# Optimization experiments

Hardware: AMD Instinct MI355X
Metric: run time of the kernel (lower is better)

The kernel has to match this reference:

```python
import jax, jax.numpy as jnp
import numpy as np
import math

B, N, DIM, NH, K, PD = 2, 2048, 512, 8, 32, 16
HD = DIM // NH
LN_EPS = 1e-6  # flax LayerNorm default


def _poincare_dist(x, y, c):
    # x, y broadcast to [B, N, N, PD]; returns [B, N, N]
    diff_norm_sq = jnp.sum((x - y) ** 2, axis=-1)
    x_norm_sq = jnp.sum(x ** 2, axis=-1)
    y_norm_sq = jnp.sum(y ** 2, axis=-1)
    den = (1.0 - c * x_norm_sq) * (1.0 - c * y_norm_sq)
    arg = 1.0 + 2.0 * c * diff_norm_sq / jnp.clip(den, 1e-8)
    safe_arg = jnp.maximum(arg, 1.0 + 1e-7)
    return jnp.arccosh(safe_arg) / jnp.sqrt(c)


def _layernorm(x, scale, bias):
    m = jnp.mean(x, axis=-1, keepdims=True)
    v = jnp.var(x, axis=-1, keepdims=True)
    return (x - m) / jnp.sqrt(v + LN_EPS) * scale + bias


def setup_inputs() -> dict:
    key = jax.random.key(0)
    ks = jax.random.split(key, 12)

    def dense(k, din, dout):
        W = jax.random.normal(k, (din, dout), jnp.float32) / np.sqrt(din).astype(np.float32)
        b = jnp.zeros((dout,), jnp.float32)
        return W, b

    inp = {}
    inp["x"] = jax.random.normal(ks[0], (B, N, DIM), jnp.float32)
    # points inside the unit Poincare ball (c=1)
    inp["positions"] = (jax.random.uniform(ks[1], (B, N, PD), jnp.float32) - 0.5) * 0.2
    inp["c"] = jnp.float32(1.0)
    inp["Wq"], inp["bq"] = dense(ks[2], DIM, DIM)
    inp["Wk"], inp["bk"] = dense(ks[3], DIM, DIM)
    inp["Wv"], inp["bv"] = dense(ks[4], DIM, DIM)
    inp["Wo"], inp["bo"] = dense(ks[5], DIM, DIM)
    inp["W1"], inp["b1"] = dense(ks[6], DIM, 4 * DIM)
    inp["W2"], inp["b2"] = dense(ks[7], 4 * DIM, DIM)
    inp["ln1_scale"] = jnp.ones((DIM,), jnp.float32)
    inp["ln1_bias"] = jnp.zeros((DIM,), jnp.float32)
    inp["ln2_scale"] = jnp.ones((DIM,), jnp.float32)
    inp["ln2_bias"] = jnp.zeros((DIM,), jnp.float32)
    inp["log_tau"] = jnp.zeros((1,), jnp.float32)
    inp["attn_scale"] = jnp.ones((1,), jnp.float32)
    return inp


def reference(x, positions, c, Wq, bq, Wk, bk, Wv, bv, Wo, bo,
              W1, b1, W2, b2, ln1_scale, ln1_bias, ln2_scale, ln2_bias,
              log_tau, attn_scale):
    x_res = x
    x_norm = _layernorm(x, ln1_scale, ln1_bias)

    def heads(W, b):
        return (x_norm @ W + b).reshape(B, N, NH, HD).transpose(0, 2, 1, 3)  # [B,H,N,HD]

    q = heads(Wq, bq)
    k = heads(Wk, bk)
    v = heads(Wv, bv)

    # pairwise hyperbolic distances [B,N,N]
    dist_matrix = _poincare_dist(positions[:, None, :, :], positions[:, :, None, :], c)
    _, top_k_indices = jax.lax.top_k(-dist_matrix, K)  # [B,N,K]

    # gather neighbor K/V: out[b,h,i,j,d] = kv[b,h, idx[b,i,j], d]
    gather = jax.vmap(lambda kv_b, idx_b: kv_b[:, idx_b, :])
    k_gathered = gather(k, top_k_indices)  # [B,H,N,K,HD]
    v_gathered = gather(v, top_k_indices)  # [B,H,N,K,HD]

    feature_scores = jnp.einsum('bhid,bhikd->bhik', q, k_gathered) / math.sqrt(HD)
    gathered_dists = jnp.take_along_axis(dist_matrix, top_k_indices, axis=-1)  # [B,N,K]
    geometric_scores = -gathered_dists[:, None, :, :] / jnp.clip(jnp.exp(log_tau), 1e-8)
    attn_scores = attn_scale * jnp.tanh(feature_scores + geometric_scores)
    attn_weights = jax.nn.softmax(attn_scores, axis=-1)

    attn_output = jnp.einsum('bhik,bhikd->bhid', attn_weights, v_gathered)
    attn_output = attn_output.transpose(0, 2, 1, 3).reshape(B, N, DIM)

    x1 = x_res + attn_output @ Wo + bo
    x2_norm = _layernorm(x1, ln2_scale, ln2_bias)
    ffn = jax.nn.gelu(x2_norm @ W1 + b1) @ W2 + b2  # gelu approximate=True (flax default)
    return x1 + ffn
```

## Files before the change

### kernel.cpp

```cpp
#include <hip/hip_runtime.h>
#include <math.h>

#define B_   2
#define N_   2048
#define DIM_ 512
#define NH_  8
#define HD_  64
#define K_   32
#define PD_  16
#define TOK_ (B_*N_)
#define FFN_ 2048
#define QKV_ (3*DIM_)
#define KV_  1024

typedef __bf16 bf16x8 __attribute__((ext_vector_type(8)));
typedef float  f32x4  __attribute__((ext_vector_type(4)));

__device__ __forceinline__ unsigned short f2bf(float f) {
    unsigned int u = __float_as_uint(f);
    u = (u + 0x7fffu + ((u >> 16) & 1u)) >> 16;
    return (unsigned short)u;
}

__device__ __forceinline__ float bflo(unsigned u) { return __uint_as_float(u << 16); }
__device__ __forceinline__ float bfhi(unsigned u) { return __uint_as_float(u & 0xffff0000u); }

__device__ __forceinline__ float gelu_tanh(float x) {
    float x3 = x * x * x;
    return 0.5f * x * (1.f + tanhf(0.7978845608028654f * (x + 0.044715f * x3)));
}

__device__ __forceinline__ float tanh_fast(float x) {
    float e = __expf(2.f * x);
    return 1.f - 2.f / (e + 1.f);
}

__device__ __forceinline__ int lane_mbcnt(unsigned long long m) {
    return __builtin_amdgcn_mbcnt_hi((unsigned)(m >> 32),
           __builtin_amdgcn_mbcnt_lo((unsigned)m, 0));
}

#define GLOAD_LDS16(g, l) __builtin_amdgcn_global_load_lds(                        \
    (const __attribute__((address_space(1))) unsigned int*)(const void*)(g),       \
    (__attribute__((address_space(3))) unsigned int*)(void*)(l), 16, 0, 0)

template<int EPI, int BM, int BN>
__global__ __launch_bounds__(256)
void gemm_bf16_kernel(const unsigned short* __restrict__ A,
                      const unsigned short* __restrict__ Bt,
                      const float* __restrict__ bias,
                      const float* __restrict__ res,
                      float* __restrict__ Cf,
                      unsigned short* __restrict__ Cb,
                      int N, int Kstride, int Kchunk)
{
    constexpr int WM = BM / 2;
    constexpr int WN = BN / 2;
    constexpr int FM = WM / 16;
    constexpr int FN = WN / 16;

    __shared__ __align__(16) unsigned short smem[(BM+BN)*64];
    unsigned short* As_ = smem;
    unsigned short* Bs_ = smem + BM * 64;

    int t    = threadIdx.x;
    int lane = t & 63;
    int wid  = t >> 6;
    int wm   = wid >> 1, wn = wid & 1;
    int bm0  = blockIdx.y * BM;
    int bn0  = blockIdx.x * BN;
    int quad = lane >> 4;
    int rlo  = lane & 15;
    int kbase = blockIdx.z * Kchunk;

    f32x4 acc[FM][FN] = {};

    for (int k0 = kbase; k0 < kbase + Kchunk; k0 += 64) {
#pragma unroll
        for (int l = 0; l < BM/32; l++) {
            int idx = l*256 + t;
            int r   = idx >> 3;
            int g   = (idx & 7) ^ (r & 7);
            GLOAD_LDS16(A + (size_t)(bm0 + r) * Kstride + k0 + g*8, As_ + idx*8);
        }
#pragma unroll
        for (int l = 0; l < BN/32; l++) {
            int idx = l*256 + t;
            int r   = idx >> 3;
            int g   = (idx & 7) ^ (r & 7);
            GLOAD_LDS16(Bt + (size_t)(bn0 + r) * Kstride + k0 + g*8, Bs_ + idx*8);
        }
        __syncthreads();

        bf16x8 af[FM][2], bfr[FN][2];
#pragma unroll
        for (int mi = 0; mi < FM; mi++) {
            int r = wm*WM + mi*16 + rlo;
#pragma unroll
            for (int s = 0; s < 2; s++)
                af[mi][s] = *(const bf16x8*)(As_ + r*64 + ((s*4 + quad) ^ (r & 7))*8);
        }
#pragma unroll
        for (int ni = 0; ni < FN; ni++) {
            int r = wn*WN + ni*16 + rlo;
#pragma unroll
            for (int s = 0; s < 2; s++)
                bfr[ni][s] = *(const bf16x8*)(Bs_ + r*64 + ((s*4 + quad) ^ (r & 7))*8);
        }
#pragma unroll
        for (int s = 0; s < 2; s++)
#pragma unroll
            for (int mi = 0; mi < FM; mi++)
#pragma unroll
                for (int ni = 0; ni < FN; ni++)
                    acc[mi][ni] = __builtin_amdgcn_mfma_f32_16x16x32_bf16(
                        af[mi][s], bfr[ni][s], acc[mi][ni], 0, 0, 0);
        __syncthreads();
    }

#pragma unroll
    for (int mi = 0; mi < FM; mi++) {
#pragma unroll
        for (int ni = 0; ni < FN; ni++) {
            int col = bn0 + wn*WN + ni*16 + rlo;
            float bv = (EPI == 4) ? 0.f : bias[col];
#pragma unroll
            for (int r = 0; r < 4; r++) {
                int row = bm0 + wm*WM + mi*16 + quad*4 + r;
                float val = acc[mi][ni][r] + bv;
                if (EPI == 1) val += res[(size_t)row * N + col];
                if (EPI == 2) {
                    val = gelu_tanh(val);
                    Cb[(size_t)row * N + col] = f2bf(val);
                } else if (EPI == 3) {
                    if (col < DIM_) Cf[(size_t)row * DIM_ + col] = val;
                    else            Cb[(size_t)row * KV_ + (col - DIM_)] = f2bf(val);
                } else if (EPI == 4) {
                    atomicAdd(&Cf[(size_t)row * N + col], val);
                } else {
                    Cf[(size_t)row * N + col] = val;
                }
            }
        }
    }
}

__device__ __forceinline__ void extract_row(const unsigned* rb, unsigned T,
                                            int cnt_lt, int m,
                                            unsigned long long* crow,
                                            int hw, int jbase, int lane)
{
    int ltpos = 0;
#pragma unroll
    for (int tt = 0; tt < 16; tt++) {
        bool is_lt = rb[tt] < T;
        unsigned long long mlt = __ballot(is_lt);
        int p = ltpos + lane_mbcnt(mlt);
        if (is_lt) {
            int j = jbase + (tt >> 2)*256 + lane*4 + (tt & 3);
            crow[hw*K_ + p] = ((unsigned long long)rb[tt] << 32) | (unsigned)j;
        }
        ltpos += __popcll(mlt);
    }
    int eqpos = 0;
#pragma unroll
    for (int jg = 0; jg < 4; jg++) {
        bool iseq[4]; unsigned long long meq[4]; int bel[4];
#pragma unroll
        for (int jj = 0; jj < 4; jj++) {
            iseq[jj] = (rb[jg*4+jj] == T);
            meq[jj]  = __ballot(iseq[jj]);
            bel[jj]  = lane_mbcnt(meq[jj]);
        }
        int lane_prefix = bel[0] + bel[1] + bel[2] + bel[3];
        int within = 0;
#pragma unroll
        for (int jj = 0; jj < 4; jj++) {
            int p = eqpos + lane_prefix + within;
            if (iseq[jj] && p < m) {
                int j = jbase + jg*256 + lane*4 + jj;
                crow[hw*K_ + cnt_lt + p] =
                    ((unsigned long long)rb[jg*4+jj] << 32) | (unsigned)j;
            }
            within += iseq[jj] ? 1 : 0;
        }
        eqpos += __popcll(meq[0]) + __popcll(meq[1]) + __popcll(meq[2]) + __popcll(meq[3]);
    }
}

__global__ __launch_bounds__(256)
void dist_topk_kernel(const float* __restrict__ pos,
                      const float* __restrict__ posT,
                      const float* __restrict__ pos_sq,
                      const float* __restrict__ c_ptr,
                      int* __restrict__ topk_idx, float* __restrict__ topk_dist)
{
    __shared__ unsigned long long cand[4][64];

    int wid  = threadIdx.x >> 6;
    int lane = threadIdx.x & 63;
    int rg   = wid >> 1;
    int hw   = wid & 1;
    int bi0  = blockIdx.x * 4 + rg * 2;
    int b    = bi0 >> 11;
    float c  = *c_ptr;
    float inv_sqrt_c = rsqrtf(c);

    float pi0[16], pi1[16];
    {
        const float4* q0 = (const float4*)(pos + (size_t)bi0 * PD_);
        const float4* q1 = (const float4*)(pos + (size_t)(bi0+1) * PD_);
#pragma unroll
        for (int u = 0; u < 4; u++) {
            float4 a = q0[u];
            pi0[4*u]=a.x; pi0[4*u+1]=a.y; pi0[4*u+2]=a.z; pi0[4*u+3]=a.w;
            float4 e = q1[u];
            pi1[4*u]=e.x; pi1[4*u+1]=e.y; pi1[4*u+2]=e.z; pi1[4*u+3]=e.w;
        }
    }
    float om0 = 1.f - c * pos_sq[bi0];
    float om1 = 1.f - c * pos_sq[bi0+1];

    const float* pT  = posT + (size_t)b * 16 * N_;
    const float* sqb = pos_sq + b * N_;
    int jbase = hw * 1024;
    int j0l   = jbase + lane * 4;

    unsigned rb0[16], rb1[16];
#pragma unroll
    for (int jg = 0; jg < 4; jg++) {
        int j0 = j0l + jg * 256;
        float ax=0,ay=0,az=0,aw=0, bx=0,by=0,bz=0,bw=0;
#pragma unroll
        for (int d = 0; d < 16; d++) {
            float4 v = *(const float4*)(pT + d * N_ + j0);
            float d0x = pi0[d]-v.x, d0y = pi0[d]-v.y, d0z = pi0[d]-v.z, d0w = pi0[d]-v.w;
            ax += d0x*d0x; ay += d0y*d0y; az += d0z*d0z; aw += d0w*d0w;
            float d1x = pi1[d]-v.x, d1y = pi1[d]-v.y, d1z = pi1[d]-v.z, d1w = pi1[d]-v.w;
            bx += d1x*d1x; by += d1y*d1y; bz += d1z*d1z; bw += d1w*d1w;
        }
        float4 sq = *(const float4*)(sqb + j0);
        float da[4]={ax,ay,az,aw}, db[4]={bx,by,bz,bw}, sqa[4]={sq.x,sq.y,sq.z,sq.w};
#pragma unroll
        for (int jj = 0; jj < 4; jj++) {
            float omj  = 1.f - c * sqa[jj];
            float den0 = fmaxf(om0 * omj, 1e-8f);
            float den1 = fmaxf(om1 * omj, 1e-8f);
            rb0[jg*4+jj] = __float_as_uint(fmaxf(1.f + 2.f*c*da[jj]/den0, 1.f+1e-7f));
            rb1[jg*4+jj] = __float_as_uint(fmaxf(1.f + 2.f*c*db[jj]/den1, 1.f+1e-7f));
        }
    }

    unsigned T0, T1;
    {
        unsigned band0 = rb0[0], bor0 = rb0[0], band1 = rb1[0], bor1 = rb1[0];
#pragma unroll
        for (int tt = 1; tt < 16; tt++) {
            band0 &= rb0[tt]; bor0 |= rb0[tt];
            band1 &= rb1[tt]; bor1 |= rb1[tt];
        }
#pragma unroll
        for (int off = 32; off; off >>= 1) {
            band0 &= __shfl_xor(band0, off); bor0 |= __shfl_xor(bor0, off);
            band1 &= __shfl_xor(band1, off); bor1 |= __shfl_xor(bor1, off);
        }
        unsigned df0 = band0 ^ bor0, df1 = band1 ^ bor1;
        int hib0 = df0 ? (31 - __clz(df0)) : -1;
        int hib1 = df1 ? (31 - __clz(df1)) : -1;
        int hib  = hib0 > hib1 ? hib0 : hib1;
        T0 = (hib >= 0) ? (band0 & ~((1u << (hib+1)) - 1u)) : band0;
        T1 = (hib >= 0) ? (band1 & ~((1u << (hib+1)) - 1u)) : band1;
        for (int bit = hib; bit >= 0; --bit) {
            unsigned p0 = T0 | (1u << bit), p1 = T1 | (1u << bit);
            int c0 = 0, c1 = 0;
#pragma unroll
            for (int tt = 0; tt < 16; tt++) {
                c0 += __popcll(__ballot(rb0[tt] < p0));
                c1 += __popcll(__ballot(rb1[tt] < p1));
            }
            if (c0 < K_) T0 = p0;
            if (c1 < K_) T1 = p1;
        }
    }
    int cl0 = 0, cl1 = 0;
#pragma unroll
    for (int tt = 0; tt < 16; tt++) {
        cl0 += __popcll(__ballot(rb0[tt] < T0));
        cl1 += __popcll(__ballot(rb1[tt] < T1));
    }

    extract_row(rb0, T0, cl0, K_ - cl0, cand[rg*2+0], hw, jbase, lane);
    extract_row(rb1, T1, cl1, K_ - cl1, cand[rg*2+1], hw, jbase, lane);
    __syncthreads();

    {
        unsigned long long mykey = cand[wid][lane];
        int rank = 0;
#pragma unroll 8
        for (int M = 0; M < 64; M++)
            rank += (cand[wid][M] < mykey) ? 1 : 0;
        if (rank < K_) {
            int bi = blockIdx.x * 4 + wid;
            topk_idx [(size_t)bi * K_ + rank] = (int)(mykey & 0xffffffffu);
            topk_dist[(size_t)bi * K_ + rank] =
                acoshf(__uint_as_float((unsigned)(mykey >> 32))) * inv_sqrt_c;
        }
    }
}

__global__ void fused_prep_kernel(const float* __restrict__ Wq, const float* __restrict__ Wk,
                            const float* __restrict__ Wv, const float* __restrict__ Wo,
                            const float* __restrict__ W1, const float* __restrict__ W2,
                            const float* __restrict__ bq, const float* __restrict__ bk,
                            const float* __restrict__ bv, const float* __restrict__ bo,
                            unsigned short* __restrict__ qkvWt,
                            unsigned short* __restrict__ WoT,
                            unsigned short* __restrict__ W1T,
                            unsigned short* __restrict__ W2T,
                            float* __restrict__ qkv_b,
                            const float* __restrict__ pos,
                            float* __restrict__ pos_sq,
                            float* __restrict__ posT,
                            const float* __restrict__ x,
                            const float* __restrict__ ln1_scale,
                            const float* __restrict__ ln1_bias,
                            unsigned short* __restrict__ xn,
                            float* __restrict__ x1)
{
    int id = blockIdx.x;
    int t  = threadIdx.x;

    if (id >= 4118) {
        int i4 = (id - 4118) * 256 + t;
        float4 xv = ((const float4*)x)[i4];
        int col4 = (i4 & 127) * 4;
        float4 bv4 = *(const float4*)(bo + col4);
        xv.x += bv4.x; xv.y += bv4.y; xv.z += bv4.z; xv.w += bv4.w;
        ((float4*)x1)[i4] = xv;
        return;
    }
    if (id >= 3094) {
        int wave = (id - 3094) * 4 + (t >> 6);
        int lane = t & 63;
        const float* xr = x + (size_t)wave * DIM_;
        float v[8];
        float s = 0.f;
#pragma unroll
        for (int i = 0; i < 8; i++) { v[i] = xr[lane + i*64]; s += v[i]; }
#pragma unroll
        for (int off = 32; off; off >>= 1) s += __shfl_xor(s, off);
        float mean = s * (1.f / DIM_);
        float vs = 0.f;
#pragma unroll
        for (int i = 0; i < 8; i++) { float d = v[i] - mean; vs += d*d; }
#pragma unroll
        for (int off = 32; off; off >>= 1) vs += __shfl_xor(vs, off);
        float inv = rsqrtf(vs * (1.f / DIM_) + 1e-6f);
        unsigned short* yr = xn + (size_t)wave * DIM_;
#pragma unroll
        for (int i = 0; i < 8; i++) {
            int cc = lane + i*64;
            yr[cc] = f2bf((v[i] - mean) * inv * ln1_scale[cc] + ln1_bias[cc]);
        }
        return;
    }
    if (id >= 3078) {
        int i = (id - 3078) * 256 + t;
        int b = i >> 11, j = i & (N_ - 1);
        const float4* p = (const float4*)(pos + (size_t)i * PD_);
        float4 a0 = p[0], a1 = p[1], a2 = p[2], a3 = p[3];
        float pv[16] = {a0.x,a0.y,a0.z,a0.w, a1.x,a1.y,a1.z,a1.w,
                        a2.x,a2.y,a2.z,a2.w, a3.x,a3.y,a3.z,a3.w};
        float s = 0.f;
#pragma unroll
        for (int d = 0; d < 16; d++) s += pv[d]*pv[d];
        pos_sq[i] = s;
        float* pT = posT + (size_t)b * 16 * N_;
#pragma unroll
        for (int d = 0; d < 16; d++) pT[d * N_ + j] = pv[d];
        return;
    }
    if (id >= 3072) {
        int i = (id - 3072) * 256 + t;
        if (i < DIM_)            qkv_b[i] = bq[i];
        else if (i < 2*DIM_)     qkv_b[i] = bk[i - DIM_];
        else                     qkv_b[i] = bv[i - 2*DIM_];
        return;
    }

    const float* W; unsigned short* Wt; int Kd, Nw, nx, ti;
    if      (id < 256)  { W = Wq; Wt = qkvWt;               Kd = 512;  Nw = 512;  nx = 16; ti = id; }
    else if (id < 512)  { W = Wk; Wt = qkvWt + 512*512;     Kd = 512;  Nw = 512;  nx = 16; ti = id - 256; }
    else if (id < 768)  { W = Wv; Wt = qkvWt + 2*512*512;   Kd = 512;  Nw = 512;  nx = 16; ti = id - 512; }
    else if (id < 1024) { W = Wo; Wt = WoT;                 Kd = 512;  Nw = 512;  nx = 16; ti = id - 768; }
    else if (id < 2048) { W = W1; Wt = W1T;                 Kd = 512;  Nw = 2048; nx = 64; ti = id - 1024; }
    else                { W = W2; Wt = W2T;                 Kd = 2048; Nw = 512;  nx = 16; ti = id - 2048; }

    __shared__ float tile[32][33];
    int n0 = (ti % nx) * 32, k0 = (ti / nx) * 32;
    int tx = t & 31, ty = t >> 5;
#pragma unroll
    for (int i = 0; i < 32; i += 8)
        tile[ty + i][tx] = W[(size_t)(k0 + ty + i) * Nw + n0 + tx];
    __syncthreads();
#pragma unroll
    for (int i = 0; i < 32; i += 8)
        Wt[(size_t)(n0 + ty + i) * Kd + k0 + tx] = f2bf(tile[tx][ty + i]);
}

__global__ void ln2_init_kernel(const float* __restrict__ x1,
                                const float* __restrict__ scale,
                                const float* __restrict__ bias,
                                const float* __restrict__ b2,
                                unsigned short* __restrict__ y,
                                float* __restrict__ outf)
{
    int wave = (blockIdx.x * blockDim.x + threadIdx.x) >> 6;
    int lane = threadIdx.x & 63;
    if (wave >= TOK_) return;
    const float* xr = x1 + (size_t)wave * DIM_;
    float v[8];
    float s = 0.f;
#pragma unroll
    for (int i = 0; i < 8; i++) { v[i] = xr[lane + i*64]; s += v[i]; }
#pragma unroll
    for (int off = 32; off; off >>= 1) s += __shfl_xor(s, off);
    float mean = s * (1.f / DIM_);
    float vs = 0.f;
#pragma unroll
    for (int i = 0; i < 8; i++) { float d = v[i] - mean; vs += d*d; }
#pragma unroll
    for (int off = 32; off; off >>= 1) vs += __shfl_xor(vs, off);
    float inv = rsqrtf(vs * (1.f / DIM_) + 1e-6f);
    unsigned short* yr = y + (size_t)wave * DIM_;
    float* orow = outf + (size_t)wave * DIM_;
#pragma unroll
    for (int i = 0; i < 8; i++) {
        int c = lane + i*64;
        yr[c] = f2bf((v[i] - mean) * inv * scale[c] + bias[c]);
        orow[c] = v[i] + b2[c];
    }
}

__global__ __launch_bounds__(256)
void attn_kernel(const float* __restrict__ q,
                 const unsigned short* __restrict__ kv,
                 const int* __restrict__ topk_idx, const float* __restrict__ topk_dist,
                 const float* __restrict__ log_tau_p, const float* __restrict__ attn_scale_p,
                 unsigned int* __restrict__ out)
{
    int gw   = (blockIdx.x * blockDim.x + threadIdx.x) >> 6;
    int lane = threadIdx.x & 63;
    if (gw >= B_ * NH_ * N_) return;
    int b = gw / (NH_ * N_);
    int r = gw % (NH_ * N_);
    int h = r / N_;
    int i = r % N_;
    int tok = b * N_ + i;

    float tau    = fmaxf(__expf(*log_tau_p), 1e-8f);
    float ascale = *attn_scale_p;

    const int*   idxp = topk_idx  + (size_t)tok * K_;
    const float* dstp = topk_dist + (size_t)tok * K_;
    int   my_idx  = idxp[lane & 31];
    float my_dist = dstp[lane & 31];

    int jj   = lane >> 1;
    int half = lane & 1;

    const float4* qp = (const float4*)(q + (size_t)tok * DIM_ + h * HD_ + half * 32);
    float4 qv[8];
#pragma unroll
    for (int u = 0; u < 8; u++) qv[u] = qp[u];

    int nb = __shfl(my_idx, jj);
    const uint4* kp = (const uint4*)(kv + (size_t)(b * N_ + nb) * KV_ + h * HD_ + half * 32);
    float dot = 0.f;
#pragma unroll
    for (int u = 0; u < 4; u++) {
        uint4 kw = kp[u];
        dot += qv[2*u].x   * bflo(kw.x) + qv[2*u].y   * bfhi(kw.x)
             + qv[2*u].z   * bflo(kw.y) + qv[2*u].w   * bfhi(kw.y)
             + qv[2*u+1].x * bflo(kw.z) + qv[2*u+1].y * bfhi(kw.z)
             + qv[2*u+1].z * bflo(kw.w) + qv[2*u+1].w * bfhi(kw.w);
    }
    dot += __shfl_xor(dot, 1);

    float fs = dot * 0.125f;
    float gs = -__shfl(my_dist, jj) / tau;
    float s  = ascale * tanh_fast(fs + gs);

    float mx = s;
#pragma unroll
    for (int off = 32; off; off >>= 1) mx = fmaxf(mx, __shfl_xor(mx, off));
    float e  = __expf(s - mx);
    float ec = half ? 0.f : e;
#pragma unroll
    for (int off = 32; off; off >>= 1) ec += __shfl_xor(ec, off);
    float inv = 1.f / ec;

    int dp    = lane & 31;
    int half2 = lane >> 5;
    const unsigned int* vb = (const unsigned int*)(kv + DIM_ + h * HD_) + dp;
    float ax = 0.f, ay = 0.f;
#pragma unroll
    for (int it = 0; it < 16; it++) {
        int t2 = half2 + 2*it;
        float w  = __shfl(e, t2 * 2) * inv;
        int   nj = __shfl(my_idx, t2);
        unsigned vv = vb[(size_t)(b * N_ + nj) * (KV_/2)];
        ax += w * bflo(vv);
        ay += w * bfhi(vv);
    }
    ax += __shfl_xor(ax, 32);
    ay += __shfl_xor(ay, 32);
    if (lane < 32) {
        unsigned pck = ((unsigned)f2bf(ay) << 16) | (unsigned)f2bf(ax);
        out[(size_t)tok * (DIM_/2) + h * (HD_/2) + dp] = pck;
    }
}

extern "C" void kernel_launch(void* const* d_in, const int* in_sizes, int n_in,
                              void* d_out, int out_size, void* d_ws, size_t ws_size,
                              hipStream_t stream)
{
    const float* x          = (const float*)d_in[0];
    const float* positions  = (const float*)d_in[1];
    const float* c_p        = (const float*)d_in[2];
    const float* Wq         = (const float*)d_in[3];
    const float* bq         = (const float*)d_in[4];
    const float* Wk         = (const float*)d_in[5];
    const float* bk         = (const float*)d_in[6];
    const float* Wv         = (const float*)d_in[7];
    const float* bv         = (const float*)d_in[8];
    const float* Wo         = (const float*)d_in[9];
    const float* bo         = (const float*)d_in[10];
    const float* W1         = (const float*)d_in[11];
    const float* b1         = (const float*)d_in[12];
    const float* W2         = (const float*)d_in[13];
    const float* b2         = (const float*)d_in[14];
    const float* ln1_scale  = (const float*)d_in[15];
    const float* ln1_bias   = (const float*)d_in[16];
    const float* ln2_scale  = (const float*)d_in[17];
    const float* ln2_bias   = (const float*)d_in[18];
    const float* log_tau    = (const float*)d_in[19];
    const float* attn_scale = (const float*)d_in[20];

    char* p = (char*)d_ws;
    unsigned short* qkvWt  = (unsigned short*)p; p += (size_t)QKV_ * DIM_ * 2;
    unsigned short* WoT    = (unsigned short*)p; p += (size_t)DIM_ * DIM_ * 2;
    unsigned short* W1T    = (unsigned short*)p; p += (size_t)FFN_ * DIM_ * 2;
    unsigned short* W2T    = (unsigned short*)p; p += (size_t)DIM_ * FFN_ * 2;
    float*          qkv_b  = (float*)p;          p += (size_t)QKV_ * 4;
    unsigned short* xn     = (unsigned short*)p; p += (size_t)TOK_ * DIM_ * 2;
    float*          qf     = (float*)p;          p += (size_t)TOK_ * DIM_ * 4;
    unsigned short* kvb    = (unsigned short*)p; p += (size_t)TOK_ * KV_ * 2;
    unsigned short* attn_o = (unsigned short*)p; p += (size_t)TOK_ * DIM_ * 2;
    float*          x1     = (float*)p;          p += (size_t)TOK_ * DIM_ * 4;
    unsigned short* x2n    = (unsigned short*)p; p += (size_t)TOK_ * DIM_ * 2;
    unsigned short* hbuf   = (unsigned short*)p; p += (size_t)TOK_ * FFN_ * 2;
    float*          pos_sq = (float*)p;          p += (size_t)TOK_ * 4;
    float*          posT   = (float*)p;          p += (size_t)B_ * 16 * N_ * 4;
    float*          tk_d   = (float*)p;          p += (size_t)TOK_ * K_ * 4;
    int*            tk_i   = (int*)p;            p += (size_t)TOK_ * K_ * 4;

    fused_prep_kernel<<<6166, 256, 0, stream>>>(Wq, Wk, Wv, Wo, W1, W2,
                                                bq, bk, bv, bo,
                                                qkvWt, WoT, W1T, W2T, qkv_b,
                                                positions, pos_sq, posT,
                                                x, ln1_scale, ln1_bias, xn, x1);

    gemm_bf16_kernel<3,64,128><<<dim3(QKV_/128, TOK_/64, 1), 256, 0, stream>>>(
        xn, qkvWt, qkv_b, nullptr, qf, kvb, QKV_, DIM_, DIM_);

    dist_topk_kernel<<<TOK_/4, 256, 0, stream>>>(positions, posT, pos_sq,
                                                 c_p, tk_i, tk_d);

    attn_kernel<<<(B_*NH_*N_)/4, 256, 0, stream>>>(qf, kvb, tk_i, tk_d,
                                                   log_tau, attn_scale,
                                                   (unsigned int*)attn_o);

    gemm_bf16_kernel<4,64,64><<<dim3(DIM_/64, TOK_/64, 2), 256, 0, stream>>>(
        attn_o, WoT, nullptr, nullptr, x1, nullptr, DIM_, DIM_, DIM_/2);

    ln2_init_kernel<<<TOK_/4, 256, 0, stream>>>(x1, ln2_scale, ln2_bias, b2,
                                                x2n, (float*)d_out);

    gemm_bf16_kernel<2,64,128><<<dim3(FFN_/128, TOK_/64, 1), 256, 0, stream>>>(
        x2n, W1T, b1, nullptr, nullptr, hbuf, FFN_, DIM_, DIM_);

    gemm_bf16_kernel<4,64,64><<<dim3(DIM_/64, TOK_/64, 4), 256, 0, stream>>>(
        hbuf, W2T, nullptr, nullptr, (float*)d_out, nullptr, DIM_, FFN_, FFN_/4);
}
```

Measured before the change: 269.7 us.

## Fold distance top-k into prep kernel and drop split-K atomic GEMMs

The distance/top-k work now runs as extra blocks of the prep kernel, which removes a separate launch along with the posT/pos_sq preprocessing. Distances are computed from dot products against row-major positions, with norms taken on the fly. The Wo and W2 GEMMs drop split-K with atomicAdd and use a direct bias-plus-residual epilogue, so the x1/output pre-initialisation passes go away. The cost is fewer blocks per GEMM (256), less parallelism, and a possible precision change in the diff-norm computation.

```diff
diff --git a/kernel.cpp b/kernel.cpp
--- a/kernel.cpp
+++ b/kernel.cpp
@@ -52,7 +52,7 @@
                       const float* __restrict__ res,
                       float* __restrict__ Cf,
                       unsigned short* __restrict__ Cb,
-                      int N, int Kstride, int Kchunk)
+                      int N, int Kd)
 {
     constexpr int WM = BM / 2;
     constexpr int WN = BN / 2;
@@ -71,24 +71,23 @@
     int bn0  = blockIdx.x * BN;
     int quad = lane >> 4;
     int rlo  = lane & 15;
-    int kbase = blockIdx.z * Kchunk;
 
     f32x4 acc[FM][FN] = {};
 
-    for (int k0 = kbase; k0 < kbase + Kchunk; k0 += 64) {
+    for (int k0 = 0; k0 < Kd; k0 += 64) {
 #pragma unroll
         for (int l = 0; l < BM/32; l++) {
             int idx = l*256 + t;
             int r   = idx >> 3;
             int g   = (idx & 7) ^ (r & 7);
-            GLOAD_LDS16(A + (size_t)(bm0 + r) * Kstride + k0 + g*8, As_ + idx*8);
+            GLOAD_LDS16(A + (size_t)(bm0 + r) * Kd + k0 + g*8, As_ + idx*8);
         }
 #pragma unroll
         for (int l = 0; l < BN/32; l++) {
             int idx = l*256 + t;
             int r   = idx >> 3;
             int g   = (idx & 7) ^ (r & 7);
-            GLOAD_LDS16(Bt + (size_t)(bn0 + r) * Kstride + k0 + g*8, Bs_ + idx*8);
+            GLOAD_LDS16(Bt + (size_t)(bn0 + r) * Kd + k0 + g*8, Bs_ + idx*8);
         }
         __syncthreads();
 
@@ -123,7 +122,7 @@
 #pragma unroll
         for (int ni = 0; ni < FN; ni++) {
             int col = bn0 + wn*WN + ni*16 + rlo;
-            float bv = (EPI == 4) ? 0.f : bias[col];
+            float bv = bias[col];
 #pragma unroll
             for (int r = 0; r < 4; r++) {
                 int row = bm0 + wm*WM + mi*16 + quad*4 + r;
@@ -135,8 +134,6 @@
                 } else if (EPI == 3) {
                     if (col < DIM_) Cf[(size_t)row * DIM_ + col] = val;
                     else            Cb[(size_t)row * KV_ + (col - DIM_)] = f2bf(val);
-                } else if (EPI == 4) {
-                    atomicAdd(&Cf[(size_t)row * N + col], val);
                 } else {
                     Cf[(size_t)row * N + col] = val;
                 }
@@ -188,23 +185,18 @@
     }
 }
 
-__global__ __launch_bounds__(256)
-void dist_topk_kernel(const float* __restrict__ pos,
-                      const float* __restrict__ posT,
-                      const float* __restrict__ pos_sq,
-                      const float* __restrict__ c_ptr,
-                      int* __restrict__ topk_idx, float* __restrict__ topk_dist)
-{
-    __shared__ unsigned long long cand[4][64];
-
+__device__ __forceinline__ void dist_topk_body(
+    unsigned long long (*cand)[64], int id,
+    const float* __restrict__ pos, float cc,
+    int* __restrict__ topk_idx, float* __restrict__ topk_dist)
+{
     int wid  = threadIdx.x >> 6;
     int lane = threadIdx.x & 63;
     int rg   = wid >> 1;
     int hw   = wid & 1;
-    int bi0  = blockIdx.x * 4 + rg * 2;
+    int bi0  = id * 4 + rg * 2;
     int b    = bi0 >> 11;
-    float c  = *c_ptr;
-    float inv_sqrt_c = rsqrtf(c);
+    float inv_sqrt_c = rsqrtf(cc);
 
     float pi0[16], pi1[16];
     {
@@ -218,36 +210,40 @@
             pi1[4*u]=e.x; pi1[4*u+1]=e.y; pi1[4*u+2]=e.z; pi1[4*u+3]=e.w;
         }
     }
-    float om0 = 1.f - c * pos_sq[bi0];
-    float om1 = 1.f - c * pos_sq[bi0+1];
-
-    const float* pT  = posT + (size_t)b * 16 * N_;
-    const float* sqb = pos_sq + b * N_;
+    float ni0 = 0.f, ni1 = 0.f;
+#pragma unroll
+    for (int d = 0; d < 16; d++) { ni0 += pi0[d]*pi0[d]; ni1 += pi1[d]*pi1[d]; }
+    float om0 = 1.f - cc * ni0;
+    float om1 = 1.f - cc * ni1;
+
+    const float* pb = pos + (size_t)b * N_ * PD_;
     int jbase = hw * 1024;
     int j0l   = jbase + lane * 4;
 
     unsigned rb0[16], rb1[16];
 #pragma unroll
     for (int jg = 0; jg < 4; jg++) {
-        int j0 = j0l + jg * 256;
-        float ax=0,ay=0,az=0,aw=0, bx=0,by=0,bz=0,bw=0;
-#pragma unroll
-        for (int d = 0; d < 16; d++) {
-            float4 v = *(const float4*)(pT + d * N_ + j0);
-            float d0x = pi0[d]-v.x, d0y = pi0[d]-v.y, d0z = pi0[d]-v.z, d0w = pi0[d]-v.w;
-            ax += d0x*d0x; ay += d0y*d0y; az += d0z*d0z; aw += d0w*d0w;
-            float d1x = pi1[d]-v.x, d1y = pi1[d]-v.y, d1z = pi1[d]-v.z, d1w = pi1[d]-v.w;
-            bx += d1x*d1x; by += d1y*d1y; bz += d1z*d1z; bw += d1w*d1w;
-        }
-        float4 sq = *(const float4*)(sqb + j0);
-        float da[4]={ax,ay,az,aw}, db[4]={bx,by,bz,bw}, sqa[4]={sq.x,sq.y,sq.z,sq.w};
 #pragma unroll
         for (int jj = 0; jj < 4; jj++) {
-            float omj  = 1.f - c * sqa[jj];
-            float den0 = fmaxf(om0 * omj, 1e-8f);
-            float den1 = fmaxf(om1 * omj, 1e-8f);
-            rb0[jg*4+jj] = __float_as_uint(fmaxf(1.f + 2.f*c*da[jj]/den0, 1.f+1e-7f));
-            rb1[jg*4+jj] = __float_as_uint(fmaxf(1.f + 2.f*c*db[jj]/den1, 1.f+1e-7f));
+            int j = j0l + jg*256 + jj;
+            const float4* pj = (const float4*)(pb + (size_t)j * PD_);
+            float4 v0 = pj[0], v1 = pj[1], v2 = pj[2], v3 = pj[3];
+            float vv[16] = {v0.x,v0.y,v0.z,v0.w, v1.x,v1.y,v1.z,v1.w,
+                            v2.x,v2.y,v2.z,v2.w, v3.x,v3.y,v3.z,v3.w};
+            float nj = 0.f, dot0 = 0.f, dot1 = 0.f;
+#pragma unroll
+            for (int d = 0; d < 16; d++) {
+                nj   += vv[d]*vv[d];
+                dot0 += pi0[d]*vv[d];
+                dot1 += pi1[d]*vv[d];
+            }
+            float omj   = 1.f - cc * nj;
+            float diff0 = ni0 + nj - 2.f*dot0;
+            float diff1 = ni1 + nj - 2.f*dot1;
+            float den0  = fmaxf(om0 * omj, 1e-8f);
+            float den1  = fmaxf(om1 * omj, 1e-8f);
+            rb0[jg*4+jj] = __float_as_uint(fmaxf(1.f + 2.f*cc*diff0/den0, 1.f+1e-7f));
+            rb1[jg*4+jj] = __float_as_uint(fmaxf(1.f + 2.f*cc*diff1/den1, 1.f+1e-7f));
         }
     }
 
@@ -300,7 +296,7 @@
         for (int M = 0; M < 64; M++)
             rank += (cand[wid][M] < mykey) ? 1 : 0;
         if (rank < K_) {
-            int bi = blockIdx.x * 4 + wid;
+            int bi = id * 4 + wid;
             topk_idx [(size_t)bi * K_ + rank] = (int)(mykey & 0xffffffffu);
             topk_dist[(size_t)bi * K_ + rank] =
                 acoshf(__uint_as_float((unsigned)(mykey >> 32))) * inv_sqrt_c;
@@ -308,39 +304,38 @@
     }
 }
 
-__global__ void fused_prep_kernel(const float* __restrict__ Wq, const float* __restrict__ Wk,
-                            const float* __restrict__ Wv, const float* __restrict__ Wo,
-                            const float* __restrict__ W1, const float* __restrict__ W2,
-                            const float* __restrict__ bq, const float* __restrict__ bk,
-                            const float* __restrict__ bv, const float* __restrict__ bo,
-                            unsigned short* __restrict__ qkvWt,
-                            unsigned short* __restrict__ WoT,
-                            unsigned short* __restrict__ W1T,
-                            unsigned short* __restrict__ W2T,
-                            float* __restrict__ qkv_b,
-                            const float* __restrict__ pos,
-                            float* __restrict__ pos_sq,
-                            float* __restrict__ posT,
-                            const float* __restrict__ x,
-                            const float* __restrict__ ln1_scale,
-                            const float* __restrict__ ln1_bias,
-                            unsigned short* __restrict__ xn,
-                            float* __restrict__ x1)
-{
+__global__ __launch_bounds__(256)
+void prep_dist_kernel(const float* __restrict__ Wq, const float* __restrict__ Wk,
+                      const float* __restrict__ Wv, const float* __restrict__ Wo,
+                      const float* __restrict__ W1, const float* __restrict__ W2,
+                      const float* __restrict__ bq, const float* __restrict__ bk,
+                      const float* __restrict__ bv,
+                      unsigned short* __restrict__ qkvWt,
+                      unsigned short* __restrict__ WoT,
+                      unsigned short* __restrict__ W1T,
+                      unsigned short* __restrict__ W2T,
+                      float* __restrict__ qkv_b,
+                      const float* __restrict__ pos,
+                      const float* __restrict__ c_ptr,
+                      int* __restrict__ tk_i, float* __restrict__ tk_d,
+                      const float* __restrict__ x,
+                      const float* __restrict__ ln1_scale,
+                      const float* __restrict__ ln1_bias,
+                      unsigned short* __restrict__ xn)
+{
+    __shared__ __align__(16) char smem_raw[4352];
     int id = blockIdx.x;
     int t  = threadIdx.x;
 
-    if (id >= 4118) {
-        int i4 = (id - 4118) * 256 + t;
-        float4 xv = ((const float4*)x)[i4];
-        int col4 = (i4 & 127) * 4;
-        float4 bv4 = *(const float4*)(bo + col4);
-        xv.x += bv4.x; xv.y += bv4.y; xv.z += bv4.z; xv.w += bv4.w;
-        ((float4*)x1)[i4] = xv;
+    if (id < 1024) {
+        dist_topk_body((unsigned long long (*)[64])smem_raw, id,
+                       pos, *c_ptr, tk_i, tk_d);
         return;
     }
-    if (id >= 3094) {
-        int wave = (id - 3094) * 4 + (t >> 6);
+    id -= 1024;
+
+    if (id >= 3078) {
+        int wave = (id - 3078) * 4 + (t >> 6);
         int lane = t & 63;
         const float* xr = x + (size_t)wave * DIM_;
         float v[8];
@@ -362,22 +357,6 @@
             int cc = lane + i*64;
             yr[cc] = f2bf((v[i] - mean) * inv * ln1_scale[cc] + ln1_bias[cc]);
         }
-        return;
-    }
-    if (id >= 3078) {
-        int i = (id - 3078) * 256 + t;
-        int b = i >> 11, j = i & (N_ - 1);
-        const float4* p = (const float4*)(pos + (size_t)i * PD_);
-        float4 a0 = p[0], a1 = p[1], a2 = p[2], a3 = p[3];
-        float pv[16] = {a0.x,a0.y,a0.z,a0.w, a1.x,a1.y,a1.z,a1.w,
-                        a2.x,a2.y,a2.z,a2.w, a3.x,a3.y,a3.z,a3.w};
-        float s = 0.f;
-#pragma unroll
-        for (int d = 0; d < 16; d++) s += pv[d]*pv[d];
-        pos_sq[i] = s;
-        float* pT = posT + (size_t)b * 16 * N_;
-#pragma unroll
-        for (int d = 0; d < 16; d++) pT[d * N_ + j] = pv[d];
         return;
     }
     if (id >= 3072) {
@@ -396,7 +375,7 @@
     else if (id < 2048) { W = W1; Wt = W1T;                 Kd = 512;  Nw = 2048; nx = 64; ti = id - 1024; }
     else                { W = W2; Wt = W2T;                 Kd = 2048; Nw = 512;  nx = 16; ti = id - 2048; }
 
-    __shared__ float tile[32][33];
+    float (*tile)[33] = (float (*)[33])smem_raw;
     int n0 = (ti % nx) * 32, k0 = (ti / nx) * 32;
     int tx = t & 31, ty = t >> 5;
 #pragma unroll
@@ -408,17 +387,15 @@
         Wt[(size_t)(n0 + ty + i) * Kd + k0 + tx] = f2bf(tile[tx][ty + i]);
 }
 
-__global__ void ln2_init_kernel(const float* __restrict__ x1,
-                                const float* __restrict__ scale,
-                                const float* __restrict__ bias,
-                                const float* __restrict__ b2,
-                                unsigned short* __restrict__ y,
-                                float* __restrict__ outf)
+__global__ void layernorm_kernel(const float* __restrict__ x,
+                                 const float* __restrict__ scale,
+                                 const float* __restrict__ bias,
+                                 unsigned short* __restrict__ y)
 {
     int wave = (blockIdx.x * blockDim.x + threadIdx.x) >> 6;
     int lane = threadIdx.x & 63;
     if (wave >= TOK_) return;
-    const float* xr = x1 + (size_t)wave * DIM_;
+    const float* xr = x + (size_t)wave * DIM_;
     float v[8];
     float s = 0.f;
 #pragma unroll
@@ -433,12 +410,10 @@
     for (int off = 32; off; off >>= 1) vs += __shfl_xor(vs, off);
     float inv = rsqrtf(vs * (1.f / DIM_) + 1e-6f);
     unsigned short* yr = y + (size_t)wave * DIM_;
-    float* orow = outf + (size_t)wave * DIM_;
 #pragma unroll
     for (int i = 0; i < 8; i++) {
         int c = lane + i*64;
         yr[c] = f2bf((v[i] - mean) * inv * scale[c] + bias[c]);
-        orow[c] = v[i] + b2[c];
     }
 }
 
@@ -560,36 +535,30 @@
     float*          x1     = (float*)p;          p += (size_t)TOK_ * DIM_ * 4;
     unsigned short* x2n    = (unsigned short*)p; p += (size_t)TOK_ * DIM_ * 2;
     unsigned short* hbuf   = (unsigned short*)p; p += (size_t)TOK_ * FFN_ * 2;
-    float*          pos_sq = (float*)p;          p += (size_t)TOK_ * 4;
-    float*          posT   = (float*)p;          p += (size_t)B_ * 16 * N_ * 4;
     float*          tk_d   = (float*)p;          p += (size_t)TOK_ * K_ * 4;
     int*            tk_i   = (int*)p;            p += (size_t)TOK_ * K_ * 4;
 
-    fused_prep_kernel<<<6166, 256, 0, stream>>>(Wq, Wk, Wv, Wo, W1, W2,
-                                                bq, bk, bv, bo,
-                                                qkvWt, WoT, W1T, W2T, qkv_b,
-                                                positions, pos_sq, posT,
-                                                x, ln1_scale, ln1_bias, xn, x1);
-
-    gemm_bf16_kernel<3,64,128><<<dim3(QKV_/128, TOK_/64, 1), 256, 0, stream>>>(
-        xn, qkvWt, qkv_b, nullptr, qf, kvb, QKV_, DIM_, DIM_);
-
-    dist_topk_kernel<<<TOK_/4, 256, 0, stream>>>(positions, posT, pos_sq,
-                                                 c_p, tk_i, tk_d);
+    prep_dist_kernel<<<5126, 256, 0, stream>>>(Wq, Wk, Wv, Wo, W1, W2,
+                                               bq, bk, bv,
+                                               qkvWt, WoT, W1T, W2T, qkv_b,
+                                               positions, c_p, tk_i, tk_d,
+                                               x, ln1_scale, ln1_bias, xn);
+
+    gemm_bf16_kernel<3,64,128><<<dim3(QKV_/128, TOK_/64), 256, 0, stream>>>(
+        xn, qkvWt, qkv_b, nullptr, qf, kvb, QKV_, DIM_);
 
     attn_kernel<<<(B_*NH_*N_)/4, 256, 0, stream>>>(qf, kvb, tk_i, tk_d,
                                                    log_tau, attn_scale,
                                                    (unsigned int*)attn_o);
 
-    gemm_bf16_kernel<4,64,64><<<dim3(DIM_/64, TOK_/64, 2), 256, 0, stream>>>(
-        attn_o, WoT, nullptr, nullptr, x1, nullptr, DIM_, DIM_, DIM_/2);
-
-    ln2_init_kernel<<<TOK_/4, 256, 0, stream>>>(x1, ln2_scale, ln2_bias, b2,
-                                                x2n, (float*)d_out);
-
-    gemm_bf16_kernel<2,64,128><<<dim3(FFN_/128, TOK_/64, 1), 256, 0, stream>>>(
-        x2n, W1T, b1, nullptr, nullptr, hbuf, FFN_, DIM_, DIM_);
-
-    gemm_bf16_kernel<4,64,64><<<dim3(DIM_/64, TOK_/64, 4), 256, 0, stream>>>(
-        hbuf, W2T, nullptr, nullptr, (float*)d_out, nullptr, DIM_, FFN_, FFN_/4);
-}
+    gemm_bf16_kernel<1,64,64><<<dim3(DIM_/64, TOK_/64), 256, 0, stream>>>(
+        attn_o, WoT, bo, x, x1, nullptr, DIM_, DIM_);
+
+    layernorm_kernel<<<TOK_/4, 256, 0, stream>>>(x1, ln2_scale, ln2_bias, x2n);
+
+    gemm_bf16_kernel<2,64,128><<<dim3(FFN_/128, TOK_/64), 256, 0, stream>>>(
+        x2n, W1T, b1, nullptr, nullptr, hbuf, FFN_, DIM_);
+
+    gemm_bf16_kernel<1,64,64><<<dim3(DIM_/64, TOK_/64), 256, 0, stream>>>(
+        hbuf, W2T, b2, x1, (float*)d_out, nullptr, DIM_, FFN_);
+}
```

Result: slower. 360.3 us (+33.6%).

## Double-buffer GEMM LDS tiles and replace split-K atomics with residual epilogue

Applied to the files above, without the earlier changes.

Adds a two-stage LDS double buffer to the bf16 GEMM so the next K-tile's global-to-LDS load is issued before computing the current tile, needing one barrier per iteration. Drops split-K with atomicAdd for the Wo and W2 projections; they now run as full-K GEMMs whose epilogue adds bias and residual directly. This removes the x1/out pre-initialisation passes from the prep and LN2 kernels. The trade-off is fewer blocks for the output GEMMs (128x8 grid), which lowers parallelism for the long-K W2 GEMM, and twice the LDS per block.

```diff
diff --git a/kernel.cpp b/kernel.cpp
--- a/kernel.cpp
+++ b/kernel.cpp
@@ -52,16 +52,15 @@
                       const float* __restrict__ res,
                       float* __restrict__ Cf,
                       unsigned short* __restrict__ Cb,
-                      int N, int Kstride, int Kchunk)
+                      int N, int Kd)
 {
     constexpr int WM = BM / 2;
     constexpr int WN = BN / 2;
     constexpr int FM = WM / 16;
     constexpr int FN = WN / 16;
-
-    __shared__ __align__(16) unsigned short smem[(BM+BN)*64];
-    unsigned short* As_ = smem;
-    unsigned short* Bs_ = smem + BM * 64;
+    constexpr int BUFSZ = (BM + BN) * 64;
+
+    __shared__ __align__(16) unsigned short smem[2 * BUFSZ];
 
     int t    = threadIdx.x;
     int lane = t & 63;
@@ -71,27 +70,31 @@
     int bn0  = blockIdx.x * BN;
     int quad = lane >> 4;
     int rlo  = lane & 15;
-    int kbase = blockIdx.z * Kchunk;
 
     f32x4 acc[FM][FN] = {};
 
-    for (int k0 = kbase; k0 < kbase + Kchunk; k0 += 64) {
+    auto stage = [&](int buf, int k0) {
+        unsigned short* As_ = smem + buf * BUFSZ;
+        unsigned short* Bs_ = As_ + BM * 64;
 #pragma unroll
         for (int l = 0; l < BM/32; l++) {
             int idx = l*256 + t;
             int r   = idx >> 3;
             int g   = (idx & 7) ^ (r & 7);
-            GLOAD_LDS16(A + (size_t)(bm0 + r) * Kstride + k0 + g*8, As_ + idx*8);
+            GLOAD_LDS16(A + (size_t)(bm0 + r) * Kd + k0 + g*8, As_ + idx*8);
         }
 #pragma unroll
         for (int l = 0; l < BN/32; l++) {
             int idx = l*256 + t;
             int r   = idx >> 3;
             int g   = (idx & 7) ^ (r & 7);
-            GLOAD_LDS16(Bt + (size_t)(bn0 + r) * Kstride + k0 + g*8, Bs_ + idx*8);
-        }
-        __syncthreads();
-
+            GLOAD_LDS16(Bt + (size_t)(bn0 + r) * Kd + k0 + g*8, Bs_ + idx*8);
+        }
+    };
+
+    auto compute = [&](int buf) {
+        unsigned short* As_ = smem + buf * BUFSZ;
+        unsigned short* Bs_ = As_ + BM * 64;
         bf16x8 af[FM][2], bfr[FN][2];
 #pragma unroll
         for (int mi = 0; mi < FM; mi++) {
@@ -115,7 +118,15 @@
                 for (int ni = 0; ni < FN; ni++)
                     acc[mi][ni] = __builtin_amdgcn_mfma_f32_16x16x32_bf16(
                         af[mi][s], bfr[ni][s], acc[mi][ni], 0, 0, 0);
+    };
+
+    stage(0, 0);
+    int buf = 0;
+    for (int k0 = 0; k0 < Kd; k0 += 64) {
         __syncthreads();
+        if (k0 + 64 < Kd) stage(buf ^ 1, k0 + 64);
+        compute(buf);
+        buf ^= 1;
     }
 
 #pragma unroll
@@ -123,7 +134,7 @@
 #pragma unroll
         for (int ni = 0; ni < FN; ni++) {
             int col = bn0 + wn*WN + ni*16 + rlo;
-            float bv = (EPI == 4) ? 0.f : bias[col];
+            float bv = bias[col];
 #pragma unroll
             for (int r = 0; r < 4; r++) {
                 int row = bm0 + wm*WM + mi*16 + quad*4 + r;
@@ -135,8 +146,6 @@
                 } else if (EPI == 3) {
                     if (col < DIM_) Cf[(size_t)row * DIM_ + col] = val;
                     else            Cb[(size_t)row * KV_ + (col - DIM_)] = f2bf(val);
-                } else if (EPI == 4) {
-                    atomicAdd(&Cf[(size_t)row * N + col], val);
                 } else {
                     Cf[(size_t)row * N + col] = val;
                 }
@@ -312,7 +321,7 @@
                             const float* __restrict__ Wv, const float* __restrict__ Wo,
                             const float* __restrict__ W1, const float* __restrict__ W2,
                             const float* __restrict__ bq, const float* __restrict__ bk,
-                            const float* __restrict__ bv, const float* __restrict__ bo,
+                            const float* __restrict__ bv,
                             unsigned short* __restrict__ qkvWt,
                             unsigned short* __restrict__ WoT,
                             unsigned short* __restrict__ W1T,
@@ -324,21 +333,11 @@
                             const float* __restrict__ x,
                             const float* __restrict__ ln1_scale,
                             const float* __restrict__ ln1_bias,
-                            unsigned short* __restrict__ xn,
-                            float* __restrict__ x1)
+                            unsigned short* __restrict__ xn)
 {
     int id = blockIdx.x;
     int t  = threadIdx.x;
 
-    if (id >= 4118) {
-        int i4 = (id - 4118) * 256 + t;
-        float4 xv = ((const float4*)x)[i4];
-        int col4 = (i4 & 127) * 4;
-        float4 bv4 = *(const float4*)(bo + col4);
-        xv.x += bv4.x; xv.y += bv4.y; xv.z += bv4.z; xv.w += bv4.w;
-        ((float4*)x1)[i4] = xv;
-        return;
-    }
     if (id >= 3094) {
         int wave = (id - 3094) * 4 + (t >> 6);
         int lane = t & 63;
@@ -408,17 +407,15 @@
         Wt[(size_t)(n0 + ty + i) * Kd + k0 + tx] = f2bf(tile[tx][ty + i]);
 }
 
-__global__ void ln2_init_kernel(const float* __restrict__ x1,
-                                const float* __restrict__ scale,
-                                const float* __restrict__ bias,
-                                const float* __restrict__ b2,
-                                unsigned short* __restrict__ y,
-                                float* __restrict__ outf)
+__global__ void layernorm_kernel(const float* __restrict__ x,
+                                 const float* __restrict__ scale,
+                                 const float* __restrict__ bias,
+                                 unsigned short* __restrict__ y)
 {
     int wave = (blockIdx.x * blockDim.x + threadIdx.x) >> 6;
     int lane = threadIdx.x & 63;
     if (wave >= TOK_) return;
-    const float* xr = x1 + (size_t)wave * DIM_;
+    const float* xr = x + (size_t)wave * DIM_;
     float v[8];
     float s = 0.f;
 #pragma unroll
@@ -433,12 +430,10 @@
     for (int off = 32; off; off >>= 1) vs += __shfl_xor(vs, off);
     float inv = rsqrtf(vs * (1.f / DIM_) + 1e-6f);
     unsigned short* yr = y + (size_t)wave * DIM_;
-    float* orow = outf + (size_t)wave * DIM_;
 #pragma unroll
     for (int i = 0; i < 8; i++) {
         int c = lane + i*64;
         yr[c] = f2bf((v[i] - mean) * inv * scale[c] + bias[c]);
-        orow[c] = v[i] + b2[c];
     }
 }
 
@@ -565,14 +560,13 @@
     float*          tk_d   = (float*)p;          p += (size_t)TOK_ * K_ * 4;
     int*            tk_i   = (int*)p;            p += (size_t)TOK_ * K_ * 4;
 
-    fused_prep_kernel<<<6166, 256, 0, stream>>>(Wq, Wk, Wv, Wo, W1, W2,
-                                                bq, bk, bv, bo,
+    fused_prep_kernel<<<4118, 256, 0, stream>>>(Wq, Wk, Wv, Wo, W1, W2, bq, bk, bv,
                                                 qkvWt, WoT, W1T, W2T, qkv_b,
                                                 positions, pos_sq, posT,
-                                                x, ln1_scale, ln1_bias, xn, x1);
-
-    gemm_bf16_kernel<3,64,128><<<dim3(QKV_/128, TOK_/64, 1), 256, 0, stream>>>(
-        xn, qkvWt, qkv_b, nullptr, qf, kvb, QKV_, DIM_, DIM_);
+                                                x, ln1_scale, ln1_bias, xn);
+
+    gemm_bf16_kernel<3,64,128><<<dim3(QKV_/128, TOK_/64), 256, 0, stream>>>(
+        xn, qkvWt, qkv_b, nullptr, qf, kvb, QKV_, DIM_);
 
     dist_topk_kernel<<<TOK_/4, 256, 0, stream>>>(positions, posT, pos_sq,
                                                  c_p, tk_i, tk_d);
@@ -581,15 +575,14 @@
                                                    log_tau, attn_scale,
                                                    (unsigned int*)attn_o);
 
-    gemm_bf16_kernel<4,64,64><<<dim3(DIM_/64, TOK_/64, 2), 256, 0, stream>>>(
-        attn_o, WoT, nullptr, nullptr, x1, nullptr, DIM_, DIM_, DIM_/2);
-
-    ln2_init_kernel<<<TOK_/4, 256, 0, stream>>>(x1, ln2_scale, ln2_bias, b2,
-                                                x2n, (float*)d_out);
-
-    gemm_bf16_kernel<2,64,128><<<dim3(FFN_/128, TOK_/64, 1), 256, 0, stream>>>(
-        x2n, W1T, b1, nullptr, nullptr, hbuf, FFN_, DIM_, DIM_);
-
-    gemm_bf16_kernel<4,64,64><<<dim3(DIM_/64, TOK_/64, 4), 256, 0, stream>>>(
-        hbuf, W2T, nullptr, nullptr, (float*)d_out, nullptr, DIM_, FFN_, FFN_/4);
-}
+    gemm_bf16_kernel<1,64,64><<<dim3(DIM_/64, TOK_/64), 256, 0, stream>>>(
+        attn_o, WoT, bo, x, x1, nullptr, DIM_, DIM_);
+
+    layernorm_kernel<<<TOK_/4, 256, 0, stream>>>(x1, ln2_scale, ln2_bias, x2n);
+
+    gemm_bf16_kernel<2,64,128><<<dim3(FFN_/128, TOK_/64), 256, 0, stream>>>(
+        x2n, W1T, b1, nullptr, nullptr, hbuf, FFN_, DIM_);
+
+    gemm_bf16_kernel<1,64,64><<<dim3(DIM_/64, TOK_/64), 256, 0, stream>>>(
+        hbuf, W2T, b2, x1, (float*)d_out, nullptr, DIM_, FFN_);
+}
```

Result: faster. 244.4 us (-9.4%).
